# Performance work log

Measured on AMD Instinct MI355X. Metric: run time of the kernel, lower is better.

Reference implementation:

```python
import jax, jax.numpy as jnp
import numpy as np

V, D, H, HD, L, F, T, B = 1024, 768, 12, 64, 8, 3072, 1024, 2
STD = 0.02
EPS = 1e-5


def setup_inputs() -> dict:
    key = jax.random.key(0)
    ks = jax.random.split(key, 8)
    n = jax.random.normal
    return {
        "input_ids": jax.random.randint(ks[0], (B, T), 0, V),
        "tok_emb": n(ks[1], (V, D), dtype=jnp.float32) * STD,   # tied with lm_head
        "pos_emb": n(ks[2], (1, T, D), dtype=jnp.float32) * STD,
        "ln1_w": jnp.ones((L, D)), "ln1_b": jnp.zeros((L, D)),
        "qkv_w": n(ks[3], (L, D, 3 * D), dtype=jnp.float32) * STD,
        "out_w": n(ks[4], (L, D, D), dtype=jnp.float32) * STD,
        "ln2_w": jnp.ones((L, D)), "ln2_b": jnp.zeros((L, D)),
        "ffn_w1": n(ks[5], (L, D, F), dtype=jnp.float32) * STD,
        "ffn_b1": jnp.zeros((L, F)),
        "ffn_w2": n(ks[6], (L, F, D), dtype=jnp.float32) * STD,
        "ffn_b2": jnp.zeros((L, D)),
        "lnf_w": jnp.ones((D,)), "lnf_b": jnp.zeros((D,)),
    }


def _layernorm(x, w, b):
    mu = x.mean(-1, keepdims=True)
    var = ((x - mu) ** 2).mean(-1, keepdims=True)
    return (x - mu) * jax.lax.rsqrt(var + EPS) * w + b


def _forward(input_ids, tok_emb, pos_emb, ln1_w, ln1_b, qkv_w, out_w,
             ln2_w, ln2_b, ffn_w1, ffn_b1, ffn_w2, ffn_b2, lnf_w, lnf_b):
    x = tok_emb[input_ids] + pos_emb[:, :T, :]          # (B, T, D)
    causal = jnp.tril(jnp.ones((T, T), dtype=bool))     # (T, T)
    neg_inf = jnp.finfo(x.dtype).min

    def block(x, p):
        l1w, l1b, qkvw, ow, l2w, l2b, w1, b1, w2, b2 = p
        h = _layernorm(x, l1w, l1b)
        qkv = h @ qkvw                                   # (B, T, 3D)
        q, k, v = jnp.split(qkv, 3, axis=-1)
        q = q.reshape(B, T, H, HD).transpose(0, 2, 1, 3)  # (B, H, T, HD)
        k = k.reshape(B, T, H, HD).transpose(0, 2, 1, 3)
        v = v.reshape(B, T, H, HD).transpose(0, 2, 1, 3)
        att = jnp.einsum('bhqd,bhkd->bhqk', q, k) * (1.0 / np.sqrt(HD))
        att = jnp.where(causal, att, neg_inf)
        att = jax.nn.softmax(att, axis=-1)
        y = jnp.einsum('bhqk,bhkd->bhqd', att, v)        # (B, H, T, HD)
        y = y.transpose(0, 2, 1, 3).reshape(B, T, D)
        x = x + y @ ow
        h = _layernorm(x, l2w, l2b)
        x = x + jax.nn.gelu(h @ w1 + b1, approximate=False) @ w2 + b2
        return x, None

    params = (ln1_w, ln1_b, qkv_w, out_w, ln2_w, ln2_b,
              ffn_w1, ffn_b1, ffn_w2, ffn_b2)
    x, _ = jax.lax.scan(block, x, params)
    x = _layernorm(x, lnf_w, lnf_b)
    return x @ tok_emb.T                                 # tied lm_head -> (B, T, V)


def reference(input_ids, tok_emb, pos_emb, ln1_w, ln1_b, qkv_w, out_w,
              ln2_w, ln2_b, ffn_w1, ffn_b1, ffn_w2, ffn_b2, lnf_w, lnf_b):
    return _forward(input_ids, tok_emb, pos_emb, ln1_w, ln1_b, qkv_w, out_w,
                    ln2_w, ln2_b, ffn_w1, ffn_b1, ffn_w2, ffn_b2, lnf_w, lnf_b)
```

## Files before the change

### kernel.cpp

```cpp
#include <hip/hip_runtime.h>
#include <hip/hip_bf16.h>
#include <math.h>

#define D_  768
#define T_  1024
#define B_  2
#define H_  12
#define HD_ 64
#define L_  8
#define F_  3072
#define V_  1024
#define M_  (B_ * T_)

typedef __bf16 bf16_t;
typedef __bf16 bf16x8 __attribute__((ext_vector_type(8)));
typedef float  f32x4  __attribute__((ext_vector_type(4)));

__device__ __forceinline__ void ld_g2l16(const bf16_t* g, bf16_t* l)
{
    __builtin_amdgcn_global_load_lds(
        (const __attribute__((address_space(1))) void*)g,
        (__attribute__((address_space(3))) void*)l,
        16, 0, 0);
}

template<int CTRL>
__device__ __forceinline__ float dpp_f32(float v)
{
    return __builtin_bit_cast(float,
        __builtin_amdgcn_update_dpp(0, __builtin_bit_cast(int, v),
                                    CTRL, 0xf, 0xf, true));
}
__device__ __forceinline__ float red16_max(float v)
{
    v = fmaxf(v, dpp_f32<0x121>(v));
    v = fmaxf(v, dpp_f32<0x122>(v));
    v = fmaxf(v, dpp_f32<0x124>(v));
    v = fmaxf(v, dpp_f32<0x128>(v));
    return v;
}
__device__ __forceinline__ float red16_sum(float v)
{
    v += dpp_f32<0x121>(v);
    v += dpp_f32<0x122>(v);
    v += dpp_f32<0x124>(v);
    v += dpp_f32<0x128>(v);
    return v;
}

__global__ __launch_bounds__(256) void embed_kernel(
    const int* __restrict__ ids, const float* __restrict__ tok,
    const float* __restrict__ pos, float* __restrict__ x)
{
    const int row = blockIdx.x;
    const int t   = row & (T_ - 1);
    const int id  = ids[row];
    const int c   = threadIdx.x;
#pragma unroll
    for (int i = 0; i < 3; ++i) {
        const int d = c + i * 256;
        x[(size_t)row * D_ + d] = tok[(size_t)id * D_ + d] + pos[(size_t)t * D_ + d];
    }
}

__global__ __launch_bounds__(256) void wtrans_kernel(
    const float* __restrict__ in, bf16_t* __restrict__ out, int K, int N)
{
    __shared__ float tile[32][33];
    const size_t loff = (size_t)blockIdx.z * K * N;
    const float* inp  = in  + loff;
    bf16_t*      outp = out + loff;
    const int n0 = blockIdx.x * 32, k0 = blockIdx.y * 32;
    const int tx = threadIdx.x & 31, ty = threadIdx.x >> 5;
#pragma unroll
    for (int i = 0; i < 4; ++i)
        tile[ty + 8 * i][tx] = inp[(size_t)(k0 + ty + 8 * i) * N + n0 + tx];
    __syncthreads();
#pragma unroll
    for (int i = 0; i < 4; ++i) {
        const int n = ty + 8 * i;
        outp[(size_t)(n0 + n) * K + k0 + tx] = (bf16_t)tile[tx][n];
    }
}

__global__ __launch_bounds__(256) void conv_kernel(
    const float* __restrict__ in, bf16_t* __restrict__ out)
{
    const int i = blockIdx.x * 1024 + threadIdx.x * 4;
    const f32x4 v = *(const f32x4*)(in + i);
#pragma unroll
    for (int j = 0; j < 4; ++j) out[i + j] = (bf16_t)v[j];
}

__device__ __forceinline__ float block_sum(float v)
{
    __shared__ float sm[4];
#pragma unroll
    for (int off = 32; off; off >>= 1) v += __shfl_down(v, off);
    if ((threadIdx.x & 63) == 0) sm[threadIdx.x >> 6] = v;
    __syncthreads();
    const float r = sm[0] + sm[1] + sm[2] + sm[3];
    __syncthreads();
    return r;
}

__global__ __launch_bounds__(256) void ln_kernel(
    const float* __restrict__ x, const float* __restrict__ w,
    const float* __restrict__ b, bf16_t* __restrict__ out)
{
    const int row = blockIdx.x;
    const float* xr = x + (size_t)row * D_;
    const int t = threadIdx.x;
    const float v0 = xr[t];
    const float v1 = xr[t + 256];
    const float v2 = xr[t + 512];
    const float mu = block_sum(v0 + v1 + v2) * (1.f / D_);
    const float d0 = v0 - mu, d1 = v1 - mu, d2 = v2 - mu;
    const float var = block_sum(d0 * d0 + d1 * d1 + d2 * d2) * (1.f / D_);
    const float rstd = rsqrtf(var + 1e-5f);
    bf16_t* o = out + (size_t)row * D_;
    o[t]       = (bf16_t)(d0 * rstd * w[t]       + b[t]);
    o[t + 256] = (bf16_t)(d1 * rstd * w[t + 256] + b[t + 256]);
    o[t + 512] = (bf16_t)(d2 * rstd * w[t + 512] + b[t + 512]);
}

template<int BN, bool RES, bool BIAS, bool GELU_, bool OUTF32>
__global__ __launch_bounds__(256) void gemm_bt(
    const bf16_t* __restrict__ A, const bf16_t* __restrict__ Bt,
    const float* __restrict__ bias, const float* __restrict__ res,
    void* __restrict__ Cp, int M, int N, int K)
{
    constexpr int BM = 64, BK = 64;
    constexpr int WN = BN / 2, NT = WN / 16;
    constexpr int AR = (BM * BK) / (256 * 8);
    constexpr int BR = (BN * BK) / (256 * 8);
    __shared__ bf16_t As[BM * BK];
    __shared__ bf16_t Bs[BN * BK];

    const int t    = threadIdx.x;
    const int wave = t >> 6, lane = t & 63;
    const int lr   = lane & 15, quad = lane >> 4;

    const int nx  = gridDim.x;
    const int nwg = nx * gridDim.y;
    int id = blockIdx.y * nx + blockIdx.x;
    id = (id & 7) * (nwg >> 3) + (id >> 3);
    const int bn0 = (id % nx) * BN, bm0 = (id / nx) * BM;

    const int wm   = wave >> 1, wn = wave & 1;

    f32x4 acc[2][NT];
#pragma unroll
    for (int i = 0; i < 2; ++i)
#pragma unroll
        for (int j = 0; j < NT; ++j) { f32x4 z = {0.f, 0.f, 0.f, 0.f}; acc[i][j] = z; }

    const bf16_t* asrc[AR];
    const bf16_t* bsrc[BR];
#pragma unroll
    for (int rnd = 0; rnd < AR; ++rnd) {
        const int p = rnd * 256 + t, row = p >> 3, c = (p & 7) ^ (row & 7);
        asrc[rnd] = A + (size_t)(bm0 + row) * K + c * 8;
    }
#pragma unroll
    for (int rnd = 0; rnd < BR; ++rnd) {
        const int p = rnd * 256 + t, row = p >> 3, c = (p & 7) ^ (row & 7);
        bsrc[rnd] = Bt + (size_t)(bn0 + row) * K + c * 8;
    }

    for (int k0 = 0; k0 < K; k0 += BK) {
        __syncthreads();
#pragma unroll
        for (int rnd = 0; rnd < AR; ++rnd)
            ld_g2l16(asrc[rnd] + k0, As + (rnd * 256 + wave * 64) * 8);
#pragma unroll
        for (int rnd = 0; rnd < BR; ++rnd)
            ld_g2l16(bsrc[rnd] + k0, Bs + (rnd * 256 + wave * 64) * 8);
        __syncthreads();

#pragma unroll
        for (int ks = 0; ks < 2; ++ks) {
            const int ch = ((quad + 4 * ks) ^ (lr & 7)) * 8;
            const bf16x8 a0 = *(const bf16x8*)(As + (wm * 32 + lr) * BK + ch);
            const bf16x8 a1 = *(const bf16x8*)(As + (wm * 32 + 16 + lr) * BK + ch);
#pragma unroll
            for (int nt = 0; nt < NT; ++nt) {
                const bf16x8 b = *(const bf16x8*)(Bs + (wn * WN + nt * 16 + lr) * BK + ch);
                acc[0][nt] = __builtin_amdgcn_mfma_f32_16x16x32_bf16(a0, b, acc[0][nt], 0, 0, 0);
                acc[1][nt] = __builtin_amdgcn_mfma_f32_16x16x32_bf16(a1, b, acc[1][nt], 0, 0, 0);
            }
        }
    }

#pragma unroll
    for (int mt = 0; mt < 2; ++mt) {
        const int mbase = bm0 + wm * 32 + mt * 16 + quad * 4;
#pragma unroll
        for (int nt = 0; nt < NT; ++nt) {
            const int n = bn0 + wn * WN + nt * 16 + lr;
            const float bv = BIAS ? bias[n] : 0.f;
#pragma unroll
            for (int r = 0; r < 4; ++r) {
                const int m = mbase + r;
                float v = acc[mt][nt][r] + bv;
                if (RES)   v += res[(size_t)m * N + n];
                if (GELU_) v = 0.5f * v * (1.f + erff(v * 0.70710678118654752f));
                if (OUTF32) ((float*)Cp)[(size_t)m * N + n] = v;
                else        ((bf16_t*)Cp)[(size_t)m * N + n] = (bf16_t)v;
            }
        }
    }
}

__global__ __launch_bounds__(256) void attn_kernel(
    const bf16_t* __restrict__ qkv, bf16_t* __restrict__ y)
{
    __shared__ bf16_t Ks[64][72];
    __shared__ bf16_t Vt[64][72];
    __shared__ bf16_t Ps[4][16][72];

    const int qt   = (int)gridDim.x - 1 - (int)blockIdx.x;
    const int q0   = qt * 64;
    const int bh   = blockIdx.y;
    const int b    = bh / H_;
    const int hh   = bh % H_;
    const int t    = threadIdx.x;
    const int wave = t >> 6;
    const int lane = t & 63;
    const int lr   = lane & 15;
    const int quad = lane >> 4;

    const size_t qg = ((size_t)b * T_ + q0 + wave * 16 + lr) * (3 * D_) + hh * HD_;
    const bf16x8 aQ0 = *(const bf16x8*)(qkv + qg + quad * 8);
    const bf16x8 aQ1 = *(const bf16x8*)(qkv + qg + 32 + quad * 8);

    const size_t rowb  = (size_t)b * T_;
    const size_t tstep = (size_t)64 * 3 * D_;
    const int    kkey  = t >> 2, kdc = (t & 3) * 8;
    const bf16_t* kptr = qkv + (rowb + kkey) * (3 * D_) + D_ + hh * HD_ + kdc;
    const bf16_t* vptr = qkv + (rowb + lane) * (3 * D_) + 2 * D_ + hh * HD_ + wave * 16;

    bf16x8 rk0 = *(const bf16x8*)(kptr);
    bf16x8 rk1 = *(const bf16x8*)(kptr + 32);
    bf16x8 rv0 = *(const bf16x8*)(vptr);
    bf16x8 rv1 = *(const bf16x8*)(vptr + 8);

    f32x4 o[4];
#pragma unroll
    for (int i = 0; i < 4; ++i) { f32x4 z = {0.f, 0.f, 0.f, 0.f}; o[i] = z; }
    float mrow[4] = {-1e30f, -1e30f, -1e30f, -1e30f};
    float lrow[4] = {0.f, 0.f, 0.f, 0.f};

    for (int kt = 0; kt <= qt; ++kt) {
        const int k_base = kt * 64;
        __syncthreads();

        *(bf16x8*)(&Ks[kkey][kdc])      = rk0;
        *(bf16x8*)(&Ks[kkey][kdc + 32]) = rk1;
#pragma unroll
        for (int i = 0; i < 8; ++i) {
            Vt[wave * 16 + i][lane]     = rv0[i];
            Vt[wave * 16 + 8 + i][lane] = rv1[i];
        }
        __syncthreads();

        if (kt < qt) {
            const bf16_t* kp = kptr + (size_t)(kt + 1) * tstep;
            const bf16_t* vp = vptr + (size_t)(kt + 1) * tstep;
            rk0 = *(const bf16x8*)(kp);
            rk1 = *(const bf16x8*)(kp + 32);
            rv0 = *(const bf16x8*)(vp);
            rv1 = *(const bf16x8*)(vp + 8);
        }

        f32x4 s[4];
#pragma unroll
        for (int i = 0; i < 4; ++i) { f32x4 z = {0.f, 0.f, 0.f, 0.f}; s[i] = z; }
#pragma unroll
        for (int nt = 0; nt < 4; ++nt) {
            bf16x8 bk0 = *(const bf16x8*)(&Ks[nt * 16 + lr][quad * 8]);
            bf16x8 bk1 = *(const bf16x8*)(&Ks[nt * 16 + lr][32 + quad * 8]);
            s[nt] = __builtin_amdgcn_mfma_f32_16x16x32_bf16(aQ0, bk0, s[nt], 0, 0, 0);
            s[nt] = __builtin_amdgcn_mfma_f32_16x16x32_bf16(aQ1, bk1, s[nt], 0, 0, 0);
        }

#pragma unroll
        for (int r = 0; r < 4; ++r) {
            const int qg_i = q0 + wave * 16 + quad * 4 + r;
            float mx = -1e30f;
#pragma unroll
            for (int nt = 0; nt < 4; ++nt) {
                float sv = s[nt][r] * 0.125f;
                if (k_base + nt * 16 + lr > qg_i) sv = -1e30f;
                s[nt][r] = sv;
                mx = fmaxf(mx, sv);
            }
            mx = red16_max(mx);
            const float mnew = fmaxf(mrow[r], mx);
            float ps = 0.f;
#pragma unroll
            for (int nt = 0; nt < 4; ++nt) {
                const float p = __expf(s[nt][r] - mnew);
                s[nt][r] = p;
                ps += p;
            }
            ps = red16_sum(ps);
            const float alpha = __expf(mrow[r] - mnew);
            lrow[r] = lrow[r] * alpha + ps;
            mrow[r] = mnew;
#pragma unroll
            for (int nt = 0; nt < 4; ++nt) o[nt][r] *= alpha;
        }

#pragma unroll
        for (int nt = 0; nt < 4; ++nt)
#pragma unroll
            for (int r = 0; r < 4; ++r)
                Ps[wave][quad * 4 + r][nt * 16 + lr] = (bf16_t)s[nt][r];

        const bf16x8 aP0 = *(const bf16x8*)(&Ps[wave][lr][quad * 8]);
        const bf16x8 aP1 = *(const bf16x8*)(&Ps[wave][lr][32 + quad * 8]);
#pragma unroll
        for (int nt = 0; nt < 4; ++nt) {
            bf16x8 bv0 = *(const bf16x8*)(&Vt[nt * 16 + lr][quad * 8]);
            bf16x8 bv1 = *(const bf16x8*)(&Vt[nt * 16 + lr][32 + quad * 8]);
            o[nt] = __builtin_amdgcn_mfma_f32_16x16x32_bf16(aP0, bv0, o[nt], 0, 0, 0);
            o[nt] = __builtin_amdgcn_mfma_f32_16x16x32_bf16(aP1, bv1, o[nt], 0, 0, 0);
        }
    }

#pragma unroll
    for (int r = 0; r < 4; ++r) {
        const float inv = 1.f / lrow[r];
        const size_t row = (size_t)b * T_ + q0 + wave * 16 + quad * 4 + r;
#pragma unroll
        for (int nt = 0; nt < 4; ++nt)
            y[row * D_ + hh * HD_ + nt * 16 + lr] = (bf16_t)(o[nt][r] * inv);
    }
}

extern "C" void kernel_launch(void* const* d_in, const int* in_sizes, int n_in,
                              void* d_out, int out_size, void* d_ws, size_t ws_size,
                              hipStream_t stream)
{
    const int*   ids  = (const int*)d_in[0];
    const float* tok  = (const float*)d_in[1];
    const float* pos  = (const float*)d_in[2];
    const float* l1w  = (const float*)d_in[3];
    const float* l1b  = (const float*)d_in[4];
    const float* qkvw = (const float*)d_in[5];
    const float* outw = (const float*)d_in[6];
    const float* l2w  = (const float*)d_in[7];
    const float* l2b  = (const float*)d_in[8];
    const float* w1   = (const float*)d_in[9];
    const float* b1   = (const float*)d_in[10];
    const float* w2   = (const float*)d_in[11];
    const float* b2   = (const float*)d_in[12];
    const float* lnfw = (const float*)d_in[13];
    const float* lnfb = (const float*)d_in[14];

    float*  x     = (float*)d_ws;
    bf16_t* h     = (bf16_t*)(x + (size_t)M_ * D_);
    bf16_t* qkv   = h     + (size_t)M_ * D_;
    bf16_t* y     = qkv   + (size_t)M_ * 3 * D_;
    bf16_t* mid   = y     + (size_t)M_ * D_;
    bf16_t* tokb  = mid   + (size_t)M_ * F_;
    bf16_t* wqkvT = tokb  + (size_t)V_ * D_;
    bf16_t* woutT = wqkvT + (size_t)L_ * 3 * D_ * D_;
    bf16_t* w1T   = woutT + (size_t)L_ * D_ * D_;
    bf16_t* w2T   = w1T   + (size_t)L_ * D_ * F_;

    embed_kernel<<<M_, 256, 0, stream>>>(ids, tok, pos, x);
    conv_kernel<<<(V_ * D_) / 1024, 256, 0, stream>>>(tok, tokb);

    wtrans_kernel<<<dim3(3 * D_ / 32, D_ / 32, L_), 256, 0, stream>>>(qkvw, wqkvT, D_, 3 * D_);
    wtrans_kernel<<<dim3(D_ / 32, D_ / 32, L_), 256, 0, stream>>>(outw, woutT, D_, D_);
    wtrans_kernel<<<dim3(F_ / 32, D_ / 32, L_), 256, 0, stream>>>(w1, w1T, D_, F_);
    wtrans_kernel<<<dim3(D_ / 32, F_ / 32, L_), 256, 0, stream>>>(w2, w2T, F_, D_);

    for (int l = 0; l < L_; ++l) {
        const bf16_t* wq  = wqkvT + (size_t)l * 3 * D_ * D_;
        const bf16_t* wo  = woutT + (size_t)l * D_ * D_;
        const bf16_t* wf1 = w1T   + (size_t)l * D_ * F_;
        const bf16_t* wf2 = w2T   + (size_t)l * F_ * D_;

        ln_kernel<<<M_, 256, 0, stream>>>(x, l1w + l * D_, l1b + l * D_, h);
        gemm_bt<128, false, false, false, false><<<dim3(3 * D_ / 128, M_ / 64), 256, 0, stream>>>(
            h, wq, nullptr, nullptr, qkv, M_, 3 * D_, D_);
        attn_kernel<<<dim3(T_ / 64, B_ * H_), 256, 0, stream>>>(qkv, y);
        gemm_bt<64, true, false, false, true><<<dim3(D_ / 64, M_ / 64), 256, 0, stream>>>(
            y, wo, nullptr, x, x, M_, D_, D_);
        ln_kernel<<<M_, 256, 0, stream>>>(x, l2w + l * D_, l2b + l * D_, h);
        gemm_bt<128, false, true, true, false><<<dim3(F_ / 128, M_ / 64), 256, 0, stream>>>(
            h, wf1, b1 + (size_t)l * F_, nullptr, mid, M_, F_, D_);
        gemm_bt<64, true, true, false, true><<<dim3(D_ / 64, M_ / 64), 256, 0, stream>>>(
            mid, wf2, b2 + (size_t)l * D_, x, x, M_, D_, F_);
    }

    ln_kernel<<<M_, 256, 0, stream>>>(x, lnfw, lnfb, h);
    gemm_bt<64, false, false, false, true><<<dim3(V_ / 64, M_ / 64), 256, 0, stream>>>(
        h, tokb, nullptr, nullptr, d_out, M_, V_, D_);
}
```

Measured before the change: 1.255 ms.

## Write V transposed from QKV GEMM epilogue and use swizzled vector LDS stores in attention

The QKV GEMM epilogue now writes the V part directly into a per-head transposed (B,H,HD,T) buffer. The attention kernel then loads V rows contiguously along T and stores them to LDS with 16-byte XOR-swizzled writes, replacing the scalar element-by-element transpose into LDS. The goal is to cut LDS write count and bank conflicts in the attention inner loop. In exchange, the GEMM epilogue does scattered 2-byte global stores strided by T for the V columns, which may be poorly coalesced.

Result: no change. 1.279 ms (+1.9%).

```diff
diff --git a/kernel.cpp b/kernel.cpp
--- a/kernel.cpp
+++ b/kernel.cpp
@@ -124,11 +124,11 @@
     o[t + 512] = (bf16_t)(d2 * rstd * w[t + 512] + b[t + 512]);
 }
 
-template<int BN, bool RES, bool BIAS, bool GELU_, bool OUTF32>
+template<int BN, bool RES, bool BIAS, bool GELU_, bool OUTF32, bool VSPLIT>
 __global__ __launch_bounds__(256) void gemm_bt(
     const bf16_t* __restrict__ A, const bf16_t* __restrict__ Bt,
     const float* __restrict__ bias, const float* __restrict__ res,
-    void* __restrict__ Cp, int M, int N, int K)
+    void* __restrict__ Cp, bf16_t* __restrict__ vTout, int M, int N, int K)
 {
     constexpr int BM = 64, BK = 64;
     constexpr int WN = BN / 2, NT = WN / 16;
@@ -147,7 +147,7 @@
     id = (id & 7) * (nwg >> 3) + (id >> 3);
     const int bn0 = (id % nx) * BN, bm0 = (id / nx) * BM;
 
-    const int wm   = wave >> 1, wn = wave & 1;
+    const int wm = wave >> 1, wn = wave & 1;
 
     f32x4 acc[2][NT];
 #pragma unroll
@@ -205,18 +205,26 @@
                 float v = acc[mt][nt][r] + bv;
                 if (RES)   v += res[(size_t)m * N + n];
                 if (GELU_) v = 0.5f * v * (1.f + erff(v * 0.70710678118654752f));
-                if (OUTF32) ((float*)Cp)[(size_t)m * N + n] = v;
-                else        ((bf16_t*)Cp)[(size_t)m * N + n] = (bf16_t)v;
+                if (VSPLIT && n >= 2 * D_) {
+                    const int np = n - 2 * D_, hh = np >> 6, dd = np & 63;
+                    const int bb = m >> 10, tt = m & 1023;
+                    vTout[(((size_t)bb * H_ + hh) * HD_ + dd) * T_ + tt] = (bf16_t)v;
+                } else if (OUTF32) {
+                    ((float*)Cp)[(size_t)m * N + n] = v;
+                } else {
+                    ((bf16_t*)Cp)[(size_t)m * N + n] = (bf16_t)v;
+                }
             }
         }
     }
 }
 
 __global__ __launch_bounds__(256) void attn_kernel(
-    const bf16_t* __restrict__ qkv, bf16_t* __restrict__ y)
+    const bf16_t* __restrict__ qkv, const bf16_t* __restrict__ vT,
+    bf16_t* __restrict__ y)
 {
     __shared__ bf16_t Ks[64][72];
-    __shared__ bf16_t Vt[64][72];
+    __shared__ bf16_t Vt2[64 * 64];
     __shared__ bf16_t Ps[4][16][72];
 
     const int qt   = (int)gridDim.x - 1 - (int)blockIdx.x;
@@ -238,12 +246,16 @@
     const size_t tstep = (size_t)64 * 3 * D_;
     const int    kkey  = t >> 2, kdc = (t & 3) * 8;
     const bf16_t* kptr = qkv + (rowb + kkey) * (3 * D_) + D_ + hh * HD_ + kdc;
-    const bf16_t* vptr = qkv + (rowb + lane) * (3 * D_) + 2 * D_ + hh * HD_ + wave * 16;
+
+    const int vrow = t >> 2, vc = t & 3;
+    const int vs0  = (2 * vc)     ^ (vrow & 7);
+    const int vs1  = (2 * vc + 1) ^ (vrow & 7);
+    const bf16_t* vptrT = vT + ((size_t)bh * HD_ + vrow) * T_ + vc * 16;
 
     bf16x8 rk0 = *(const bf16x8*)(kptr);
     bf16x8 rk1 = *(const bf16x8*)(kptr + 32);
-    bf16x8 rv0 = *(const bf16x8*)(vptr);
-    bf16x8 rv1 = *(const bf16x8*)(vptr + 8);
+    bf16x8 rv0 = *(const bf16x8*)(vptrT);
+    bf16x8 rv1 = *(const bf16x8*)(vptrT + 8);
 
     f32x4 o[4];
 #pragma unroll
@@ -257,16 +269,13 @@
 
         *(bf16x8*)(&Ks[kkey][kdc])      = rk0;
         *(bf16x8*)(&Ks[kkey][kdc + 32]) = rk1;
-#pragma unroll
-        for (int i = 0; i < 8; ++i) {
-            Vt[wave * 16 + i][lane]     = rv0[i];
-            Vt[wave * 16 + 8 + i][lane] = rv1[i];
-        }
+        *(bf16x8*)(&Vt2[vrow * 64 + vs0 * 8]) = rv0;
+        *(bf16x8*)(&Vt2[vrow * 64 + vs1 * 8]) = rv1;
         __syncthreads();
 
         if (kt < qt) {
             const bf16_t* kp = kptr + (size_t)(kt + 1) * tstep;
-            const bf16_t* vp = vptr + (size_t)(kt + 1) * tstep;
+            const bf16_t* vp = vptrT + (size_t)(kt + 1) * 64;
             rk0 = *(const bf16x8*)(kp);
             rk1 = *(const bf16x8*)(kp + 32);
             rv0 = *(const bf16x8*)(vp);
@@ -322,8 +331,9 @@
         const bf16x8 aP1 = *(const bf16x8*)(&Ps[wave][lr][32 + quad * 8]);
 #pragma unroll
         for (int nt = 0; nt < 4; ++nt) {
-            bf16x8 bv0 = *(const bf16x8*)(&Vt[nt * 16 + lr][quad * 8]);
-            bf16x8 bv1 = *(const bf16x8*)(&Vt[nt * 16 + lr][32 + quad * 8]);
+            const int vr = (nt * 16 + lr) * 64;
+            bf16x8 bv0 = *(const bf16x8*)(&Vt2[vr + ((quad     ^ (lr & 7))) * 8]);
+            bf16x8 bv1 = *(const bf16x8*)(&Vt2[vr + (((quad+4) ^ (lr & 7))) * 8]);
             o[nt] = __builtin_amdgcn_mfma_f32_16x16x32_bf16(aP0, bv0, o[nt], 0, 0, 0);
             o[nt] = __builtin_amdgcn_mfma_f32_16x16x32_bf16(aP1, bv1, o[nt], 0, 0, 0);
         }
@@ -369,6 +379,7 @@
     bf16_t* woutT = wqkvT + (size_t)L_ * 3 * D_ * D_;
     bf16_t* w1T   = woutT + (size_t)L_ * D_ * D_;
     bf16_t* w2T   = w1T   + (size_t)L_ * D_ * F_;
+    bf16_t* vT    = w2T   + (size_t)L_ * F_ * D_;
 
     embed_kernel<<<M_, 256, 0, stream>>>(ids, tok, pos, x);
     conv_kernel<<<(V_ * D_) / 1024, 256, 0, stream>>>(tok, tokb);
@@ -385,19 +396,19 @@
         const bf16_t* wf2 = w2T   + (size_t)l * F_ * D_;
 
         ln_kernel<<<M_, 256, 0, stream>>>(x, l1w + l * D_, l1b + l * D_, h);
-        gemm_bt<128, false, false, false, false><<<dim3(3 * D_ / 128, M_ / 64), 256, 0, stream>>>(
-            h, wq, nullptr, nullptr, qkv, M_, 3 * D_, D_);
-        attn_kernel<<<dim3(T_ / 64, B_ * H_), 256, 0, stream>>>(qkv, y);
-        gemm_bt<64, true, false, false, true><<<dim3(D_ / 64, M_ / 64), 256, 0, stream>>>(
-            y, wo, nullptr, x, x, M_, D_, D_);
+        gemm_bt<128, false, false, false, false, true><<<dim3(3 * D_ / 128, M_ / 64), 256, 0, stream>>>(
+            h, wq, nullptr, nullptr, qkv, vT, M_, 3 * D_, D_);
+        attn_kernel<<<dim3(T_ / 64, B_ * H_), 256, 0, stream>>>(qkv, vT, y);
+        gemm_bt<64, true, false, false, true, false><<<dim3(D_ / 64, M_ / 64), 256, 0, stream>>>(
+            y, wo, nullptr, x, x, nullptr, M_, D_, D_);
         ln_kernel<<<M_, 256, 0, stream>>>(x, l2w + l * D_, l2b + l * D_, h);
-        gemm_bt<128, false, true, true, false><<<dim3(F_ / 128, M_ / 64), 256, 0, stream>>>(
-            h, wf1, b1 + (size_t)l * F_, nullptr, mid, M_, F_, D_);
-        gemm_bt<64, true, true, false, true><<<dim3(D_ / 64, M_ / 64), 256, 0, stream>>>(
-            mid, wf2, b2 + (size_t)l * D_, x, x, M_, D_, F_);
+        gemm_bt<128, false, true, true, false, false><<<dim3(F_ / 128, M_ / 64), 256, 0, stream>>>(
+            h, wf1, b1 + (size_t)l * F_, nullptr, mid, nullptr, M_, F_, D_);
+        gemm_bt<64, true, true, false, true, false><<<dim3(D_ / 64, M_ / 64), 256, 0, stream>>>(
+            mid, wf2, b2 + (size_t)l * D_, x, x, nullptr, M_, D_, F_);
     }
 
     ln_kernel<<<M_, 256, 0, stream>>>(x, lnfw, lnfb, h);
-    gemm_bt<64, false, false, false, true><<<dim3(V_ / 64, M_ / 64), 256, 0, stream>>>(
-        h, tokb, nullptr, nullptr, d_out, M_, V_, D_);
-}
+    gemm_bt<64, false, false, false, true, false><<<dim3(V_ / 64, M_ / 64), 256, 0, stream>>>(
+        h, tokb, nullptr, nullptr, d_out, nullptr, M_, V_, D_);
+}
```
